# Optimization experiments

Measured on AMD Instinct MI355X. Metric: run time of the kernel, lower is better.

Reference implementation:

```python
import jax, jax.numpy as jnp
import numpy as np

DIM = 2048
HID = 1024
E = 16
TOP_K = 2
S_SHARED = 2


def setup_inputs() -> dict:
    key = jax.random.key(0)
    ks = jax.random.split(key, 6)
    scale = 0.02
    x = jax.random.normal(ks[0], (2, 2048, DIM), dtype=jnp.float32)
    gate_w = jax.random.normal(ks[1], (DIM, E), dtype=jnp.float32) * scale
    shared_w1 = jax.random.normal(ks[2], (S_SHARED, DIM, HID), dtype=jnp.float32) * scale
    shared_w2 = jax.random.normal(ks[3], (S_SHARED, HID, DIM), dtype=jnp.float32) * scale
    w1 = jax.random.normal(ks[4], (E, DIM, HID), dtype=jnp.float32) * scale
    w2 = jax.random.normal(ks[5], (E, HID, DIM), dtype=jnp.float32) * scale
    return {"x": x, "gate_w": gate_w, "shared_w1": shared_w1,
            "shared_w2": shared_w2, "w1": w1, "w2": w2}


def reference(x, gate_w, shared_w1, shared_w2, w1, w2):
    orig_shape = x.shape
    xf = x.reshape(-1, orig_shape[-1])  # [T, D]

    # Shared experts: sum of SiLU MLPs
    hs = jax.nn.silu(jnp.einsum('td,sdh->sth', xf, shared_w1))
    shared_out = jnp.einsum('sth,shd->td', hs, shared_w2)

    # Gating
    probs = jax.nn.softmax(xf @ gate_w, axis=-1)              # [T, E]
    weights, indices = jax.lax.top_k(probs, TOP_K)            # [T, K]
    weights = weights / weights.sum(axis=-1, keepdims=True)
    aux_loss = (probs.mean(axis=0) ** 2).sum() * E

    # Combine weights per (token, expert): top_k indices are distinct
    combine = (jax.nn.one_hot(indices, E, dtype=xf.dtype) *
               weights[..., None]).sum(axis=1)                # [T, E]

    # Dense all-expert compute (reference form of gather-GEMM-scatter)
    h = jax.nn.silu(jnp.einsum('td,edh->eth', xf, w1))        # [E, T, H]
    y = jnp.einsum('eth,ehd->etd', h, w2)                     # [E, T, D]
    routed_out = jnp.einsum('te,etd->td', combine, y)         # [T, D]

    out = (shared_out + routed_out).reshape(orig_shape)
    return out, aux_loss
```

## Files before the change

### kernel.cpp

```cpp
#include <hip/hip_runtime.h>
#include <math.h>

typedef unsigned short u16;
typedef __bf16 bf16x8 __attribute__((ext_vector_type(8)));
typedef float f32x4 __attribute__((ext_vector_type(4)));

#define T_TOK 4096
#define DIMD 2048
#define HIDD 1024
#define NEXP 16
#define RMAX 10240
#define MAXBLK 96
#define BM 128
#define BN 128
#define BK 32
#define LDK 40

__device__ __forceinline__ u16 f2b(float f) {
  unsigned u = __builtin_bit_cast(unsigned, f);
  unsigned r = (u + 0x7FFFu + ((u >> 16) & 1u)) >> 16;
  return (u16)r;
}


__global__ void k_init(int* perm, int* cnt, int* fill) {
  int i = blockIdx.x * blockDim.x + threadIdx.x;
  if (i < RMAX) perm[i] = -1;
  if (i < NEXP) { cnt[i] = 0; fill[i] = 0; }
}

__global__ void k_cvt(const float* __restrict__ x, u16* __restrict__ xb) {
  const int i = blockIdx.x * blockDim.x + threadIdx.x;
  const float4 v = ((const float4*)x)[i];
  union { u16 u[4]; unsigned long long q; } t;
  t.u[0] = f2b(v.x); t.u[1] = f2b(v.y); t.u[2] = f2b(v.z); t.u[3] = f2b(v.w);
  ((unsigned long long*)xb)[i] = t.q;
}

__global__ __launch_bounds__(256)
void k_gate(const float* __restrict__ x, const float* __restrict__ gw,
            int* __restrict__ top2i, float* __restrict__ top2w,
            int* __restrict__ cnt, float* __restrict__ partial) {
  const int e = threadIdx.x & 15;
  const int tt = threadIdx.x >> 4;
  const int t = blockIdx.x * 16 + tt;
  const float* xp = x + (size_t)t * DIMD;
  float acc = 0.f;
#pragma unroll 8
  for (int k = 0; k < DIMD; ++k) acc = fmaf(xp[k], gw[k * NEXP + e], acc);
  __shared__ float lg[16][17];
  __shared__ float pr[16][17];
  lg[tt][e] = acc;
  __syncthreads();
  if (e == 0) {
    float l[16];
    float mx = -1e30f;
    for (int j = 0; j < 16; ++j) { l[j] = lg[tt][j]; mx = fmaxf(mx, l[j]); }
    float s = 0.f;
    for (int j = 0; j < 16; ++j) { l[j] = expf(l[j] - mx); s += l[j]; }
    const float inv = 1.f / s;
    float p1 = -1.f, p2 = -1.f; int i1 = 0, i2 = 0;
    for (int j = 0; j < 16; ++j) {
      const float p = l[j] * inv;
      pr[tt][j] = p;
      if (p > p1) { p2 = p1; i2 = i1; p1 = p; i1 = j; }
      else if (p > p2) { p2 = p; i2 = j; }
    }
    const float wsum = p1 + p2;
    top2i[t * 2 + 0] = i1;
    top2i[t * 2 + 1] = i2;
    top2w[t * 2 + 0] = p1 / wsum;
    top2w[t * 2 + 1] = p2 / wsum;
    atomicAdd(&cnt[i1], 1);
    atomicAdd(&cnt[i2], 1);
  }
  __syncthreads();
  if (tt == 0) {
    float s = 0.f;
    for (int j = 0; j < 16; ++j) s += pr[j][e];
    partial[blockIdx.x * 16 + e] = s;
  }
}

__global__ __launch_bounds__(256)
void k_aux(const float* __restrict__ partial, float* __restrict__ auxOut) {
  __shared__ float s[16][17];
  const int e = threadIdx.x & 15, c = threadIdx.x >> 4;
  float a = 0.f;
  for (int b = c; b < 256; b += 16) a += partial[b * 16 + e];
  s[c][e] = a;
  __syncthreads();
  if (threadIdx.x == 0) {
    float aux = 0.f;
    for (int j = 0; j < 16; ++j) {
      float tot = 0.f;
      for (int cc = 0; cc < 16; ++cc) tot += s[cc][j];
      const float m = tot / (float)T_TOK;
      aux += m * m;
    }
    auxOut[0] = aux * (float)NEXP;
  }
}

__global__ void k_off(const int* __restrict__ cnt, int* __restrict__ offs,
                      int* __restrict__ tbl_e, int* __restrict__ tbl_r0,
                      int* __restrict__ nblk) {
  if (threadIdx.x != 0 || blockIdx.x != 0) return;
  int o = 0, nb = 0;
  for (int e = 0; e < NEXP; ++e) {
    offs[e] = o;
    const int b = (cnt[e] + BM - 1) / BM;
    for (int i = 0; i < b; ++i) { tbl_e[nb] = e; tbl_r0[nb] = o + i * BM; ++nb; }
    o += b * BM;
  }
  offs[NEXP] = o;
  nblk[0] = nb;
}

__global__ void k_fill(const int* __restrict__ top2i, const float* __restrict__ top2w,
                       const int* __restrict__ offs, int* __restrict__ fill,
                       int* __restrict__ perm, float* __restrict__ wrow) {
  const int id = blockIdx.x * blockDim.x + threadIdx.x;
  if (id >= T_TOK * 2) return;
  const int e = top2i[id];
  const int pos = atomicAdd(&fill[e], 1);
  const int r = offs[e] + pos;
  perm[r] = id >> 1;
  wrow[r] = top2w[id];
}

template<int MODE>
__global__ __launch_bounds__(256)
void k_gemm(const u16* __restrict__ A, const float* __restrict__ Bg,
            void* __restrict__ Outp,
            const int* __restrict__ perm, const float* __restrict__ wrow,
            const int* __restrict__ tbl_e, const int* __restrict__ tbl_r0,
            const int* __restrict__ nblk,
            int K, int lda, int ldb) {
  __shared__ u16 As[BM * LDK];
  __shared__ u16 Bs[BN * LDK];
  __shared__ int rowIdxS[BM];

  const int bx = blockIdx.x, by = blockIdx.y;
  int expert = 0;
  int r0;
  if (MODE == 2 || MODE == 3) {
    if (bx >= *nblk) return;
    expert = tbl_e[bx];
    r0 = tbl_r0[bx];
  } else {
    r0 = bx * BM;
    if (MODE == 0) expert = blockIdx.z;
  }
  const float* B = Bg + (size_t)expert * (size_t)K * (size_t)ldb;

  const int tid = threadIdx.x;
  if (tid < BM) {
    int r = r0 + tid;
    int rowi = r;
    if (MODE == 2) { int p = perm[r]; rowi = (p < 0) ? 0 : p; }
    rowIdxS[tid] = rowi;
  }
  __syncthreads();

  f32x4 acc[4][4];
#pragma unroll
  for (int i = 0; i < 4; ++i)
#pragma unroll
    for (int j = 0; j < 4; ++j) {
      acc[i][j][0] = 0.f; acc[i][j][1] = 0.f; acc[i][j][2] = 0.f; acc[i][j][3] = 0.f;
    }

  const int n0 = by * BN;
  const int aRow = tid >> 2;
  const int aQ = (tid & 3) * 8;
  const int bNN = tid & 127;
  const int bK0 = (tid >> 7) * 8;

  const int lane = tid & 63;
  const int wv = tid >> 6;
  const int wr = (wv >> 1) * 64;
  const int wc = (wv & 1) * 64;
  const int lm = lane & 15;
  const int lq = lane >> 4;

  const u16* aRd = &As[(wr + lm) * LDK + lq * 8];
  const u16* bRd = &Bs[(wc + lm) * LDK + lq * 8];
  const u16* arow0 = A + (size_t)rowIdxS[aRow] * lda + aQ;
  const u16* arow1 = A + (size_t)rowIdxS[aRow + 64] * lda + aQ;

  for (int k0 = 0; k0 < K; k0 += BK) {
    *(int4*)&As[aRow * LDK + aQ] = *(const int4*)(arow0 + k0);
    *(int4*)&As[(aRow + 64) * LDK + aQ] = *(const int4*)(arow1 + k0);
#pragma unroll
    for (int it = 0; it < 2; ++it) {
      const int kk = bK0 + it * 16;
      const float* g = B + (size_t)(k0 + kk) * ldb + n0 + bNN;
      union { u16 u[8]; int4 v; } tmp;
#pragma unroll
      for (int j = 0; j < 8; ++j) tmp.u[j] = f2b(g[(size_t)j * ldb]);
      *(int4*)&Bs[bNN * LDK + kk] = tmp.v;
    }
    __syncthreads();
    bf16x8 af[4], bq[4];
#pragma unroll
    for (int i = 0; i < 4; ++i) af[i] = *(const bf16x8*)(aRd + i * 16 * LDK);
#pragma unroll
    for (int j = 0; j < 4; ++j) bq[j] = *(const bf16x8*)(bRd + j * 16 * LDK);
#pragma unroll
    for (int i = 0; i < 4; ++i)
#pragma unroll
      for (int j = 0; j < 4; ++j)
        acc[i][j] = __builtin_amdgcn_mfma_f32_16x16x32_bf16(af[i], bq[j], acc[i][j], 0, 0, 0);
    __syncthreads();
  }

  u16* outB16 = (u16*)Outp;
  float* outF = (float*)Outp;
#pragma unroll
  for (int i = 0; i < 4; ++i) {
    const int lr0 = wr + i * 16 + lq * 4;
#pragma unroll
    for (int j = 0; j < 4; ++j) {
      const int gc = n0 + wc + j * 16 + lm;
#pragma unroll
      for (int r = 0; r < 4; ++r) {
        const float v = acc[i][j][r];
        const int lr = lr0 + r;
        if (MODE == 0) {
          const float s = v / (1.f + expf(-v));
          outB16[(size_t)(r0 + lr) * DIMD + expert * HIDD + gc] = f2b(s);
        } else if (MODE == 2) {
          const float s = v / (1.f + expf(-v));
          outB16[(size_t)(r0 + lr) * HIDD + gc] = f2b(s);
        } else if (MODE == 1) {
          outF[(size_t)(r0 + lr) * DIMD + gc] = v;
        } else {
          const int rr = r0 + lr;
          const int t = perm[rr];
          if (t >= 0) atomicAdd(&outF[(size_t)t * DIMD + gc], wrow[rr] * v);
        }
      }
    }
  }
}


extern "C" void kernel_launch(void* const* d_in, const int* in_sizes, int n_in,
                              void* d_out, int out_size, void* d_ws, size_t ws_size,
                              hipStream_t stream) {
  const float* x   = (const float*)d_in[0];
  const float* gw  = (const float*)d_in[1];
  const float* sw1 = (const float*)d_in[2];
  const float* sw2 = (const float*)d_in[3];
  const float* w1  = (const float*)d_in[4];
  const float* w2  = (const float*)d_in[5];
  float* out = (float*)d_out;

  char* ws = (char*)d_ws;
  u16* xb  = (u16*)(ws);
  u16* hbS = (u16*)(ws + (size_t)(16 << 20));
  u16* hbR = (u16*)(ws + (size_t)(32 << 20));
  char* p  = ws + (size_t)(52 << 20);
  int*   top2i   = (int*)p;    p += T_TOK * 2 * 4;
  float* top2w   = (float*)p;  p += T_TOK * 2 * 4;
  int*   perm    = (int*)p;    p += RMAX * 4;
  float* wrow    = (float*)p;  p += RMAX * 4;
  int*   cnt     = (int*)p;    p += 16 * 4;
  int*   fill    = (int*)p;    p += 16 * 4;
  int*   offs    = (int*)p;    p += 32 * 4;
  int*   tbl_e   = (int*)p;    p += MAXBLK * 4;
  int*   tbl_r0  = (int*)p;    p += MAXBLK * 4;
  int*   nblk    = (int*)p;    p += 16 * 4;
  float* partial = (float*)p;  p += 256 * 16 * 4;

  k_init<<<(RMAX + 255) / 256, 256, 0, stream>>>(perm, cnt, fill);
  k_cvt<<<(T_TOK * DIMD / 4) / 256, 256, 0, stream>>>(x, xb);
  k_gate<<<T_TOK / 16, 256, 0, stream>>>(x, gw, top2i, top2w, cnt, partial);
  k_off<<<1, 64, 0, stream>>>(cnt, offs, tbl_e, tbl_r0, nblk);
  k_fill<<<(T_TOK * 2 + 255) / 256, 256, 0, stream>>>(top2i, top2w, offs, fill, perm, wrow);
  k_aux<<<1, 256, 0, stream>>>(partial, out + (size_t)T_TOK * DIMD);

  k_gemm<0><<<dim3(32, 8, 2), 256, 0, stream>>>(xb, sw1, hbS,
      nullptr, nullptr, nullptr, nullptr, nullptr, 2048, 2048, 1024);
  k_gemm<1><<<dim3(32, 16, 1), 256, 0, stream>>>(hbS, sw2, out,
      nullptr, nullptr, nullptr, nullptr, nullptr, 2048, 2048, 2048);
  k_gemm<2><<<dim3(80, 8, 1), 256, 0, stream>>>(xb, w1, hbR,
      perm, nullptr, tbl_e, tbl_r0, nblk, 2048, 2048, 1024);
  k_gemm<3><<<dim3(80, 16, 1), 256, 0, stream>>>(hbR, w2, out,
      perm, wrow, tbl_e, tbl_r0, nblk, 1024, 1024, 2048);
}
```

Baseline: 915.8 us.

## Pre-transpose weights to bf16 and load GEMM tiles with direct global-to-LDS loads

Adds a transpose-and-convert kernel that writes every weight matrix as K-contiguous bf16 once per call. This removes the strided fp32 loads and per-element conversion inside the GEMM inner loop. The GEMM now fills its LDS tiles with global_load_lds 16-byte transfers and drops the LDK padding, which may bring back LDS bank conflicts. The cost is an extra pass that reads all fp32 weights and writes bf16 copies, plus more workspace.

```diff
diff --git a/kernel.cpp b/kernel.cpp
--- a/kernel.cpp
+++ b/kernel.cpp
@@ -14,12 +14,17 @@
 #define BM 128
 #define BN 128
 #define BK 32
-#define LDK 40
 
 __device__ __forceinline__ u16 f2b(float f) {
   unsigned u = __builtin_bit_cast(unsigned, f);
   unsigned r = (u + 0x7FFFu + ((u >> 16) & 1u)) >> 16;
   return (u16)r;
+}
+
+__device__ __forceinline__ void gld16(const void* g, void* l) {
+  __builtin_amdgcn_global_load_lds(
+      (const __attribute__((address_space(1))) void*)g,
+      (__attribute__((address_space(3))) void*)l, 16, 0, 0);
 }
 
 
@@ -35,6 +40,33 @@
   union { u16 u[4]; unsigned long long q; } t;
   t.u[0] = f2b(v.x); t.u[1] = f2b(v.y); t.u[2] = f2b(v.z); t.u[3] = f2b(v.w);
   ((unsigned long long*)xb)[i] = t.q;
+}
+
+__global__ __launch_bounds__(256)
+void k_tr(const float* __restrict__ W, u16* __restrict__ Wt,
+          int K, int N, long estride, int ld_out) {
+  __shared__ float t[64][65];
+  const int e = blockIdx.z;
+  const float* Win = W + (size_t)e * (size_t)K * (size_t)N;
+  u16* Wo = Wt + (size_t)e * (size_t)estride;
+  const int n0 = blockIdx.x * 64, k0 = blockIdx.y * 64;
+  const int r = threadIdx.x >> 4;
+  const int c = (threadIdx.x & 15) * 4;
+#pragma unroll
+  for (int p = 0; p < 4; ++p) {
+    const int kk = p * 16 + r;
+    const float4 v = *(const float4*)&Win[(size_t)(k0 + kk) * N + n0 + c];
+    t[kk][c] = v.x; t[kk][c + 1] = v.y; t[kk][c + 2] = v.z; t[kk][c + 3] = v.w;
+  }
+  __syncthreads();
+#pragma unroll
+  for (int p = 0; p < 4; ++p) {
+    const int nn = p * 16 + r;
+    ushort4 o;
+    o.x = f2b(t[c + 0][nn]); o.y = f2b(t[c + 1][nn]);
+    o.z = f2b(t[c + 2][nn]); o.w = f2b(t[c + 3][nn]);
+    *(ushort4*)&Wo[(size_t)(n0 + nn) * ld_out + k0 + c] = o;
+  }
 }
 
 __global__ __launch_bounds__(256)
@@ -131,19 +163,17 @@
 
 template<int MODE>
 __global__ __launch_bounds__(256)
-void k_gemm(const u16* __restrict__ A, const float* __restrict__ Bg,
+void k_gemm(const u16* __restrict__ A, const u16* __restrict__ Bt,
             void* __restrict__ Outp,
             const int* __restrict__ perm, const float* __restrict__ wrow,
             const int* __restrict__ tbl_e, const int* __restrict__ tbl_r0,
             const int* __restrict__ nblk,
-            int K, int lda, int ldb) {
-  __shared__ u16 As[BM * LDK];
-  __shared__ u16 Bs[BN * LDK];
-  __shared__ int rowIdxS[BM];
+            int K, int lda, int ldb, size_t bstride) {
+  __shared__ u16 As[BM * BK];
+  __shared__ u16 Bs[BN * BK];
 
   const int bx = blockIdx.x, by = blockIdx.y;
-  int expert = 0;
-  int r0;
+  int expert = 0, r0;
   if (MODE == 2 || MODE == 3) {
     if (bx >= *nblk) return;
     expert = tbl_e[bx];
@@ -152,16 +182,27 @@
     r0 = bx * BM;
     if (MODE == 0) expert = blockIdx.z;
   }
-  const float* B = Bg + (size_t)expert * (size_t)K * (size_t)ldb;
+  const u16* B = Bt + (size_t)expert * bstride;
 
   const int tid = threadIdx.x;
-  if (tid < BM) {
-    int r = r0 + tid;
-    int rowi = r;
-    if (MODE == 2) { int p = perm[r]; rowi = (p < 0) ? 0 : p; }
-    rowIdxS[tid] = rowi;
-  }
-  __syncthreads();
+  const int w = tid >> 6, lane = tid & 63;
+  const int lr = lane >> 2;
+  const int lk = (lane & 3) * 8;
+
+  int ra0 = r0 + w * 32 + lr, ra1 = ra0 + 16;
+  if (MODE == 2) {
+    const int p0 = perm[ra0]; ra0 = (p0 < 0) ? 0 : p0;
+    const int p1 = perm[ra1]; ra1 = (p1 < 0) ? 0 : p1;
+  }
+  const int n0 = by * BN;
+  const u16* ap0 = A + (size_t)ra0 * lda + lk;
+  const u16* ap1 = A + (size_t)ra1 * lda + lk;
+  const u16* bp0 = B + (size_t)(n0 + w * 32 + lr) * ldb + lk;
+  const u16* bp1 = bp0 + (size_t)16 * ldb;
+  u16* lA0 = &As[w * 1024];
+  u16* lA1 = &As[w * 1024 + 512];
+  u16* lB0 = &Bs[w * 1024];
+  u16* lB1 = &Bs[w * 1024 + 512];
 
   f32x4 acc[4][4];
 #pragma unroll
@@ -171,42 +212,22 @@
       acc[i][j][0] = 0.f; acc[i][j][1] = 0.f; acc[i][j][2] = 0.f; acc[i][j][3] = 0.f;
     }
 
-  const int n0 = by * BN;
-  const int aRow = tid >> 2;
-  const int aQ = (tid & 3) * 8;
-  const int bNN = tid & 127;
-  const int bK0 = (tid >> 7) * 8;
-
-  const int lane = tid & 63;
-  const int wv = tid >> 6;
-  const int wr = (wv >> 1) * 64;
-  const int wc = (wv & 1) * 64;
-  const int lm = lane & 15;
-  const int lq = lane >> 4;
-
-  const u16* aRd = &As[(wr + lm) * LDK + lq * 8];
-  const u16* bRd = &Bs[(wc + lm) * LDK + lq * 8];
-  const u16* arow0 = A + (size_t)rowIdxS[aRow] * lda + aQ;
-  const u16* arow1 = A + (size_t)rowIdxS[aRow + 64] * lda + aQ;
+  const int wr = (w >> 1) * 64, wc = (w & 1) * 64;
+  const int lm = lane & 15, lq = lane >> 4;
+  const u16* aRd = &As[(wr + lm) * BK + lq * 8];
+  const u16* bRd = &Bs[(wc + lm) * BK + lq * 8];
 
   for (int k0 = 0; k0 < K; k0 += BK) {
-    *(int4*)&As[aRow * LDK + aQ] = *(const int4*)(arow0 + k0);
-    *(int4*)&As[(aRow + 64) * LDK + aQ] = *(const int4*)(arow1 + k0);
-#pragma unroll
-    for (int it = 0; it < 2; ++it) {
-      const int kk = bK0 + it * 16;
-      const float* g = B + (size_t)(k0 + kk) * ldb + n0 + bNN;
-      union { u16 u[8]; int4 v; } tmp;
-#pragma unroll
-      for (int j = 0; j < 8; ++j) tmp.u[j] = f2b(g[(size_t)j * ldb]);
-      *(int4*)&Bs[bNN * LDK + kk] = tmp.v;
-    }
+    gld16(ap0 + k0, lA0);
+    gld16(ap1 + k0, lA1);
+    gld16(bp0 + k0, lB0);
+    gld16(bp1 + k0, lB1);
     __syncthreads();
     bf16x8 af[4], bq[4];
 #pragma unroll
-    for (int i = 0; i < 4; ++i) af[i] = *(const bf16x8*)(aRd + i * 16 * LDK);
-#pragma unroll
-    for (int j = 0; j < 4; ++j) bq[j] = *(const bf16x8*)(bRd + j * 16 * LDK);
+    for (int i = 0; i < 4; ++i) af[i] = *(const bf16x8*)(aRd + i * 16 * BK);
+#pragma unroll
+    for (int j = 0; j < 4; ++j) bq[j] = *(const bf16x8*)(bRd + j * 16 * BK);
 #pragma unroll
     for (int i = 0; i < 4; ++i)
 #pragma unroll
@@ -226,17 +247,17 @@
 #pragma unroll
       for (int r = 0; r < 4; ++r) {
         const float v = acc[i][j][r];
-        const int lr = lr0 + r;
+        const int lrow = lr0 + r;
         if (MODE == 0) {
           const float s = v / (1.f + expf(-v));
-          outB16[(size_t)(r0 + lr) * DIMD + expert * HIDD + gc] = f2b(s);
+          outB16[(size_t)(r0 + lrow) * DIMD + expert * HIDD + gc] = f2b(s);
         } else if (MODE == 2) {
           const float s = v / (1.f + expf(-v));
-          outB16[(size_t)(r0 + lr) * HIDD + gc] = f2b(s);
+          outB16[(size_t)(r0 + lrow) * HIDD + gc] = f2b(s);
         } else if (MODE == 1) {
-          outF[(size_t)(r0 + lr) * DIMD + gc] = v;
+          outF[(size_t)(r0 + lrow) * DIMD + gc] = v;
         } else {
-          const int rr = r0 + lr;
+          const int rr = r0 + lrow;
           const int t = perm[rr];
           if (t >= 0) atomicAdd(&outF[(size_t)t * DIMD + gc], wrow[rr] * v);
         }
@@ -258,10 +279,14 @@
   float* out = (float*)d_out;
 
   char* ws = (char*)d_ws;
-  u16* xb  = (u16*)(ws);
-  u16* hbS = (u16*)(ws + (size_t)(16 << 20));
-  u16* hbR = (u16*)(ws + (size_t)(32 << 20));
-  char* p  = ws + (size_t)(52 << 20);
+  u16* xb    = (u16*)(ws);
+  u16* hbS   = (u16*)(ws + (size_t)( 16 << 20));
+  u16* hbR   = (u16*)(ws + (size_t)( 32 << 20));
+  u16* sw1t  = (u16*)(ws + (size_t)( 52 << 20));
+  u16* sw2ct = (u16*)(ws + (size_t)( 60 << 20));
+  u16* w1t   = (u16*)(ws + (size_t)( 68 << 20));
+  u16* w2t   = (u16*)(ws + (size_t)(132 << 20));
+  char* p = ws + (size_t)(196 << 20);
   int*   top2i   = (int*)p;    p += T_TOK * 2 * 4;
   float* top2w   = (float*)p;  p += T_TOK * 2 * 4;
   int*   perm    = (int*)p;    p += RMAX * 4;
@@ -281,12 +306,17 @@
   k_fill<<<(T_TOK * 2 + 255) / 256, 256, 0, stream>>>(top2i, top2w, offs, fill, perm, wrow);
   k_aux<<<1, 256, 0, stream>>>(partial, out + (size_t)T_TOK * DIMD);
 
-  k_gemm<0><<<dim3(32, 8, 2), 256, 0, stream>>>(xb, sw1, hbS,
-      nullptr, nullptr, nullptr, nullptr, nullptr, 2048, 2048, 1024);
-  k_gemm<1><<<dim3(32, 16, 1), 256, 0, stream>>>(hbS, sw2, out,
-      nullptr, nullptr, nullptr, nullptr, nullptr, 2048, 2048, 2048);
-  k_gemm<2><<<dim3(80, 8, 1), 256, 0, stream>>>(xb, w1, hbR,
-      perm, nullptr, tbl_e, tbl_r0, nblk, 2048, 2048, 1024);
-  k_gemm<3><<<dim3(80, 16, 1), 256, 0, stream>>>(hbR, w2, out,
-      perm, wrow, tbl_e, tbl_r0, nblk, 1024, 1024, 2048);
-}
+  k_tr<<<dim3(1024 / 64, 2048 / 64,  2), 256, 0, stream>>>(sw1, sw1t, 2048, 1024, 1024l * 2048, 2048);
+  k_tr<<<dim3(2048 / 64, 1024 / 64,  2), 256, 0, stream>>>(sw2, sw2ct, 1024, 2048, 1024, 2048);
+  k_tr<<<dim3(1024 / 64, 2048 / 64, 16), 256, 0, stream>>>(w1, w1t, 2048, 1024, 1024l * 2048, 2048);
+  k_tr<<<dim3(2048 / 64, 1024 / 64, 16), 256, 0, stream>>>(w2, w2t, 1024, 2048, 2048l * 1024, 1024);
+
+  k_gemm<0><<<dim3(32, 8, 2), 256, 0, stream>>>(xb, sw1t, hbS,
+      nullptr, nullptr, nullptr, nullptr, nullptr, 2048, 2048, 2048, (size_t)1024 * 2048);
+  k_gemm<1><<<dim3(32, 16, 1), 256, 0, stream>>>(hbS, sw2ct, out,
+      nullptr, nullptr, nullptr, nullptr, nullptr, 2048, 2048, 2048, 0);
+  k_gemm<2><<<dim3(80, 8, 1), 256, 0, stream>>>(xb, w1t, hbR,
+      perm, nullptr, tbl_e, tbl_r0, nblk, 2048, 2048, 2048, (size_t)1024 * 2048);
+  k_gemm<3><<<dim3(80, 16, 1), 256, 0, stream>>>(hbR, w2t, out,
+      perm, wrow, tbl_e, tbl_r0, nblk, 1024, 1024, 1024, (size_t)2048 * 1024);
+}
```

Result: faster. 858.3 us (-6.3%).
